# Kernel tuning notes

Hardware: AMD Instinct MI355X
Metric: run time of the kernel (lower is better)

The kernel has to match this reference:

```python
import jax, jax.numpy as jnp
import numpy as np

B, T, C = 8, 4096, 1024
NH = 64          # module sets self.n_head = dim_head = 64
HD = C // NH     # 16


def setup_inputs() -> dict:
    key = jax.random.key(0)
    ks = jax.random.split(key, 9)
    s = 1.0 / np.sqrt(C).astype(np.float32)
    x = jax.random.normal(ks[0], (B, T, C), jnp.float32)
    Wq = jax.random.normal(ks[1], (C, C), jnp.float32) * s
    bq = jax.random.normal(ks[2], (C,), jnp.float32) * 0.01
    Wk = jax.random.normal(ks[3], (C, C), jnp.float32) * s
    bk = jax.random.normal(ks[4], (C,), jnp.float32) * 0.01
    Wv = jax.random.normal(ks[5], (C, C), jnp.float32) * s
    bv = jax.random.normal(ks[6], (C,), jnp.float32) * 0.01
    Wp = jax.random.normal(ks[7], (C, C), jnp.float32) * s
    bp = jax.random.normal(ks[8], (C,), jnp.float32) * 0.01
    return {"x": x, "Wq": Wq, "bq": bq, "Wk": Wk, "bk": bk,
            "Wv": Wv, "bv": bv, "Wp": Wp, "bp": bp}


def _heads(t):
    # [B, T, C] -> [B, NH, T, HD]
    return t.reshape(B, T, NH, HD).transpose(0, 2, 1, 3)


def reference(x, Wq, bq, Wk, bk, Wv, bv, Wp, bp):
    # self-attention path: y = x; kv_mask=None (masked path is unreachable in source)
    q = _heads(x @ Wq.T + bq)
    k = _heads(x @ Wk.T + bk)
    v = _heads(x @ Wv.T + bv)
    q = jax.nn.softmax(q, axis=-1)
    k = jax.nn.softmax(k, axis=-1)
    k_cumsum = k.sum(axis=2, keepdims=True)               # [B, NH, 1, HD]
    D_inv = 1.0 / (q * k_cumsum).sum(axis=-1, keepdims=True)  # [B, NH, T, 1]
    context = jnp.einsum('bhtd,bhte->bhde', k, v)          # [B, NH, HD, HD]
    y = jnp.einsum('bhtd,bhde->bhte', q, context) * D_inv  # [B, NH, T, HD]
    y = y.transpose(0, 2, 1, 3).reshape(B, T, C)           # b h n d -> b n (h d)
    return y @ Wp.T + bp
```

## Files before the change

kernel.cpp:

```cpp
#include <hip/hip_runtime.h>
#include <stdint.h>


typedef __attribute__((ext_vector_type(8))) __bf16 bf16x8;
typedef __attribute__((ext_vector_type(4))) float f32x4;
typedef __attribute__((ext_vector_type(4))) unsigned int u32x4;
typedef __attribute__((ext_vector_type(4))) unsigned short u16x4;

#define AS1 __attribute__((address_space(1)))
#define AS3 __attribute__((address_space(3)))

__device__ __forceinline__ unsigned short f2bf(float f) {
  unsigned int u = __builtin_bit_cast(unsigned int, f);
  u += 0x7FFFu + ((u >> 16) & 1u);
  return (unsigned short)(u >> 16);
}

__device__ __forceinline__ void gl_lds16(const unsigned short* g, unsigned short* l) {
  __builtin_amdgcn_global_load_lds((const AS1 unsigned int*)g, (AS3 unsigned int*)l, 16, 0, 0);
}

__global__ __launch_bounds__(256)
void cvt_all(const float* __restrict__ x,
             const float* __restrict__ w0, const float* __restrict__ w1,
             const float* __restrict__ w2, const float* __restrict__ w3,
             unsigned short* __restrict__ xb, unsigned short* __restrict__ wb) {
  const int blk = blockIdx.x;
  if (blk < 2048) {
    int i = blk * 256 + threadIdx.x;
    #pragma unroll 4
    for (; i < 8388608; i += 524288) {
      f32x4 v = *(const f32x4*)(x + (size_t)i * 4);
      u16x4 o;
      o.x = f2bf(v.x); o.y = f2bf(v.y); o.z = f2bf(v.z); o.w = f2bf(v.w);
      *(u16x4*)(xb + (size_t)i * 4) = o;
    }
  } else {
    const int g = (blk - 2048) * 256 + threadIdx.x;
    const int w = g >> 17;
    const int r = g & 131071;
    const int f = r >> 6;
    const int l = r & 63;
    const int n = (f >> 5) * 16 + (l & 15);
    const int k = (f & 31) * 32 + (l >> 4) * 8;
    const float* ws[4] = {w0, w1, w2, w3};
    const float* src = ws[w] + (size_t)n * 1024 + k;
    f32x4 v0 = *(const f32x4*)src;
    f32x4 v1 = *(const f32x4*)(src + 4);
    u16x4 a, b;
    a.x = f2bf(v0.x); a.y = f2bf(v0.y); a.z = f2bf(v0.z); a.w = f2bf(v0.w);
    b.x = f2bf(v1.x); b.y = f2bf(v1.y); b.z = f2bf(v1.z); b.w = f2bf(v1.w);
    unsigned short* o = wb + (size_t)g * 8;
    *(u16x4*)o = a;
    *(u16x4*)(o + 4) = b;
  }
}

template<int KIND>
__global__ __launch_bounds__(256, 3)
void gemm_pipe(const unsigned short* __restrict__ A,
               const unsigned short* __restrict__ Wf,
               const float* __restrict__ b0, const float* __restrict__ b1,
               const float* __restrict__ b2,
               unsigned short* __restrict__ oq, unsigned short* __restrict__ okT,
               unsigned short* __restrict__ ovT, float* __restrict__ of)
{
  __shared__ __align__(16) unsigned short lds[24576];

  const int tid  = threadIdx.x;
  const int lane = tid & 63;
  const int wid  = tid >> 6;

  const int flat  = blockIdx.x;
  const int xcd   = flat & 7;
  const int i     = flat >> 3;
  const int bcg   = i >> 8;
  const int r     = i & 255;
  const int panel = r >> 3;
  const int c     = r & 7;
  const int brow  = (xcd * 32 + panel) * 128;
  const int bcol  = (bcg * 8 + c) * 128;

  const int srow = wid * 16 + (lane >> 2);
  const int scol = ((lane & 3) ^ ((lane >> 3) & 3)) << 3;
  const unsigned short* a_src = A + (size_t)(brow + srow) * 1024 + scol;
  unsigned short* Ldst = lds + wid * 512;

  const int wm = (wid >> 1) * 64;
  const int wn = (wid & 1) * 64;
  const int fr = lane & 15;
  const int fg = lane >> 4;
  const int aoff = (wm + fr) * 32 + ((fg ^ ((fr >> 1) & 3)) << 3);

  const unsigned short* wfp = Wf + ((size_t)((bcol + wn) >> 4) * 32) * 512 + lane * 8;

  const f32x4 fz = {0.f, 0.f, 0.f, 0.f};
  f32x4 acc[4][4];
  #pragma unroll
  for (int mt = 0; mt < 4; ++mt)
    #pragma unroll
    for (int nt = 0; nt < 4; ++nt) acc[mt][nt] = fz;

  auto stage = [&](int T, int sb) {
    unsigned short* d = Ldst + sb * 8192;
    const unsigned short* g = a_src + T * 64;
    gl_lds16(g,              d);
    gl_lds16(g + 65536,      d + 2048);
    gl_lds16(g + 32,         d + 4096);
    gl_lds16(g + 65536 + 32, d + 6144);
  };
  auto loadB = [&](int k32, bf16x8 (&dst)[4]) {
    #pragma unroll
    for (int nt = 0; nt < 4; ++nt)
      dst[nt] = __builtin_bit_cast(bf16x8,
        *(const u32x4*)(wfp + (size_t)k32 * 512 + (size_t)nt * 16384));
  };

  bf16x8 bEven[4], bOdd[4];

  stage(0, 0); stage(1, 1);
  loadB(0, bEven);
  asm volatile("s_waitcnt vmcnt(8)" ::: "memory");
  __builtin_amdgcn_sched_barrier(0);
  __builtin_amdgcn_s_barrier();

  for (int T = 0; T < 16; ++T) {
    const unsigned short* Lb = lds + (T % 3) * 8192;
    bf16x8 af[8];
    #pragma unroll
    for (int mt = 0; mt < 4; ++mt) {
      af[mt]     = __builtin_bit_cast(bf16x8, *(const u32x4*)&Lb[aoff + mt * 512]);
      af[4 + mt] = __builtin_bit_cast(bf16x8, *(const u32x4*)&Lb[4096 + aoff + mt * 512]);
    }
    asm volatile("s_waitcnt lgkmcnt(0)" ::: "memory");
    __builtin_amdgcn_sched_barrier(0);
    if (T + 2 < 16) stage(T + 2, (T + 2) % 3);
    loadB(2 * T + 1, bOdd);
    if (T <= 13)      asm volatile("s_waitcnt vmcnt(8)" ::: "memory");
    else              asm volatile("s_waitcnt vmcnt(4)" ::: "memory");
    __builtin_amdgcn_sched_barrier(0);
    if (T < 15) __builtin_amdgcn_s_barrier();

    __builtin_amdgcn_s_setprio(1);
    #pragma unroll
    for (int mt = 0; mt < 4; ++mt)
      #pragma unroll
      for (int nt = 0; nt < 4; ++nt)
        acc[mt][nt] = __builtin_amdgcn_mfma_f32_16x16x32_bf16(af[mt], bEven[nt], acc[mt][nt], 0, 0, 0);
    __builtin_amdgcn_s_setprio(0);

    if (T <= 14) loadB(2 * T + 2, bEven);
    if (T <= 13)      asm volatile("s_waitcnt vmcnt(8)" ::: "memory");
    else if (T == 14) asm volatile("s_waitcnt vmcnt(4)" ::: "memory");
    else              asm volatile("s_waitcnt vmcnt(0)" ::: "memory");
    __builtin_amdgcn_sched_barrier(0);

    __builtin_amdgcn_s_setprio(1);
    #pragma unroll
    for (int mt = 0; mt < 4; ++mt)
      #pragma unroll
      for (int nt = 0; nt < 4; ++nt)
        acc[mt][nt] = __builtin_amdgcn_mfma_f32_16x16x32_bf16(af[4 + mt], bOdd[nt], acc[mt][nt], 0, 0, 0);
    __builtin_amdgcn_s_setprio(0);
  }

  const int sec = (KIND == 0) ? (bcol >> 10) : 0;
  const float* bias = (KIND == 1) ? b0 : (sec == 0 ? b0 : (sec == 1 ? b1 : b2));

  #pragma unroll
  for (int nt = 0; nt < 4; ++nt) {
    const int n_glob = bcol + wn + nt * 16 + fr;
    const int nn = (KIND == 0) ? (n_glob & 1023) : n_glob;
    const float bv = bias[nn];
    #pragma unroll
    for (int mt = 0; mt < 4; ++mt) {
      const int m0 = brow + wm + mt * 16 + fg * 4;
      float vals[4];
      #pragma unroll
      for (int r2 = 0; r2 < 4; ++r2) vals[r2] = acc[mt][nt][r2] + bv;

      if (KIND == 0 && sec <= 1) {
        #pragma unroll
        for (int r2 = 0; r2 < 4; ++r2) {
          float e = __expf(vals[r2]);
          float sm = e;
          #pragma unroll
          for (int s = 1; s < 16; s <<= 1) sm += __shfl_xor(sm, s, 64);
          vals[r2] = e * __builtin_amdgcn_rcpf(sm);
        }
      }

      if (KIND == 1) {
        #pragma unroll
        for (int r2 = 0; r2 < 4; ++r2)
          of[(size_t)(m0 + r2) * 1024 + n_glob] = vals[r2];
      } else if (sec == 0) {
        #pragma unroll
        for (int r2 = 0; r2 < 4; ++r2)
          oq[(size_t)(m0 + r2) * 1024 + nn] = f2bf(vals[r2]);
      } else {
        unsigned short* o = (sec == 1) ? okT : ovT;
        const int bb = m0 >> 12;
        const int t0 = m0 & 4095;
        const int hh = nn >> 4;
        const int dd = nn & 15;
        u16x4 pk;
        pk.x = f2bf(vals[0]); pk.y = f2bf(vals[1]);
        pk.z = f2bf(vals[2]); pk.w = f2bf(vals[3]);
        *(u16x4*)&o[(((size_t)bb * 64 + hh) * 16 + dd) * 4096 + t0] = pk;
      }
    }
  }
}

__global__ __launch_bounds__(256)
void attn_kernel(const unsigned short* __restrict__ qb,
                 const unsigned short* __restrict__ kT,
                 const unsigned short* __restrict__ vT,
                 unsigned short* __restrict__ yb)
{
  const int pair = blockIdx.x;
  const int b    = pair >> 5;
  const int hp   = pair & 31;
  const int tid  = threadIdx.x;
  const int lane = tid & 63;
  const int wid  = tid >> 6;
  const int fr   = lane & 15;
  const int fg   = lane >> 4;

  const unsigned short* kT0 = kT + ((size_t)(b * 64 + hp * 2) * 16) * 4096;
  const unsigned short* vT0 = vT + ((size_t)(b * 64 + hp * 2) * 16) * 4096;
  const unsigned short* kT1 = kT0 + 16 * 4096;
  const unsigned short* vT1 = vT0 + 16 * 4096;

  const u32x4 uz = {0u, 0u, 0u, 0u};
  const f32x4 fz = {0.f, 0.f, 0.f, 0.f};
  const u32x4 uo = {0x3F803F80u, 0x3F803F80u, 0x3F803F80u, 0x3F803F80u};
  const bf16x8 ones = __builtin_bit_cast(bf16x8, uo);

  f32x4 cctx0 = fz, ckc0 = fz, cctx1 = fz, ckc1 = fz;
  #pragma unroll 2
  for (int t0 = wid * 1024; t0 < (wid + 1) * 1024; t0 += 32) {
    const size_t off = (size_t)fr * 4096 + t0 + fg * 8;
    bf16x8 ak0 = __builtin_bit_cast(bf16x8, *(const u32x4*)&kT0[off]);
    bf16x8 bv0 = __builtin_bit_cast(bf16x8, *(const u32x4*)&vT0[off]);
    bf16x8 ak1 = __builtin_bit_cast(bf16x8, *(const u32x4*)&kT1[off]);
    bf16x8 bv1 = __builtin_bit_cast(bf16x8, *(const u32x4*)&vT1[off]);
    cctx0 = __builtin_amdgcn_mfma_f32_16x16x32_bf16(ak0, bv0, cctx0, 0, 0, 0);
    ckc0  = __builtin_amdgcn_mfma_f32_16x16x32_bf16(ak0, ones, ckc0, 0, 0, 0);
    cctx1 = __builtin_amdgcn_mfma_f32_16x16x32_bf16(ak1, bv1, cctx1, 0, 0, 0);
    ckc1  = __builtin_amdgcn_mfma_f32_16x16x32_bf16(ak1, ones, ckc1, 0, 0, 0);
  }

  __shared__ float red[4][2][16][16];
  __shared__ float kcr[4][2][16];
  __shared__ float ctxf[2][16][16];
  __shared__ float kcf[2][16];

  #pragma unroll
  for (int r = 0; r < 4; ++r) {
    red[wid][0][fg * 4 + r][fr] = cctx0[r];
    red[wid][1][fg * 4 + r][fr] = cctx1[r];
  }
  if (fr == 0) {
    #pragma unroll
    for (int r = 0; r < 4; ++r) {
      kcr[wid][0][fg * 4 + r] = ckc0[r];
      kcr[wid][1][fg * 4 + r] = ckc1[r];
    }
  }
  __syncthreads();
  {
    const int d = (tid >> 4) & 15, e = tid & 15;
    #pragma unroll
    for (int hh = 0; hh < 2; ++hh)
      ctxf[hh][d][e] = red[0][hh][d][e] + red[1][hh][d][e] + red[2][hh][d][e] + red[3][hh][d][e];
    if (tid < 32) {
      const int hh = tid >> 4, dd = tid & 15;
      kcf[hh][dd] = kcr[0][hh][dd] + kcr[1][hh][dd] + kcr[2][hh][dd] + kcr[3][hh][dd];
    }
  }
  __syncthreads();

  bf16x8 bctx0 = __builtin_bit_cast(bf16x8, uz);
  bf16x8 bctx1 = __builtin_bit_cast(bf16x8, uz);
  bf16x8 bkc0  = __builtin_bit_cast(bf16x8, uz);
  bf16x8 bkc1  = __builtin_bit_cast(bf16x8, uz);
  if (fg < 2) {
    #pragma unroll
    for (int j = 0; j < 8; ++j) {
      const int d = fg * 8 + j;
      bctx0[j] = (__bf16)ctxf[0][d][fr];
      bkc0[j]  = (__bf16)kcf[0][d];
    }
  } else {
    #pragma unroll
    for (int j = 0; j < 8; ++j) {
      const int d = (fg - 2) * 8 + j;
      bctx1[j] = (__bf16)ctxf[1][d][fr];
      bkc1[j]  = (__bf16)kcf[1][d];
    }
  }

  const size_t cbase = (size_t)b * 4096 * 1024 + (size_t)hp * 32;

  for (int step = 0; step < 64; ++step) {
    const int t0 = step * 64 + wid * 16;
    bf16x8 af = __builtin_bit_cast(bf16x8,
        *(const u32x4*)&qb[cbase + (size_t)(t0 + fr) * 1024 + fg * 8]);
    f32x4 cy0 = __builtin_amdgcn_mfma_f32_16x16x32_bf16(af, bctx0, fz, 0, 0, 0);
    f32x4 cy1 = __builtin_amdgcn_mfma_f32_16x16x32_bf16(af, bctx1, fz, 0, 0, 0);
    f32x4 cd0 = __builtin_amdgcn_mfma_f32_16x16x32_bf16(af, bkc0,  fz, 0, 0, 0);
    f32x4 cd1 = __builtin_amdgcn_mfma_f32_16x16x32_bf16(af, bkc1,  fz, 0, 0, 0);
    #pragma unroll
    for (int r = 0; r < 4; ++r) {
      const int t = t0 + fg * 4 + r;
      const size_t o = cbase + (size_t)t * 1024;
      yb[o + fr]      = f2bf(cy0[r] * __builtin_amdgcn_rcpf(cd0[r]));
      yb[o + 16 + fr] = f2bf(cy1[r] * __builtin_amdgcn_rcpf(cd1[r]));
    }
  }
}

extern "C" void kernel_launch(void* const* d_in, const int* in_sizes, int n_in,
                              void* d_out, int out_size, void* d_ws, size_t ws_size,
                              hipStream_t stream)
{
  (void)in_sizes; (void)n_in; (void)out_size; (void)ws_size;
  const float* x  = (const float*)d_in[0];
  const float* Wq = (const float*)d_in[1];
  const float* bq = (const float*)d_in[2];
  const float* Wk = (const float*)d_in[3];
  const float* bk = (const float*)d_in[4];
  const float* Wv = (const float*)d_in[5];
  const float* bv = (const float*)d_in[6];
  const float* Wp = (const float*)d_in[7];
  const float* bp = (const float*)d_in[8];

  char* ws = (char*)d_ws;
  unsigned short* xb  = (unsigned short*)(ws);
  unsigned short* wb  = (unsigned short*)(ws + 67108864);
  unsigned short* qb  = (unsigned short*)(ws + 75497472);
  unsigned short* kTb = (unsigned short*)(ws + 142606336);
  unsigned short* vTb = (unsigned short*)(ws + 209715200);

  cvt_all<<<4096, 256, 0, stream>>>(x, Wq, Wk, Wv, Wp, xb, wb);

  gemm_pipe<0><<<6144, 256, 0, stream>>>(xb, wb, bq, bk, bv, qb, kTb, vTb, nullptr);

  attn_kernel<<<256, 256, 0, stream>>>(qb, kTb, vTb, xb );

  gemm_pipe<1><<<2048, 256, 0, stream>>>(xb , wb + 3145728, bp, bp, bp,
                                         nullptr, nullptr, nullptr, (float*)d_out);
}
```

Measured before the change: 453.2 us.

## Switch projection GEMMs from 16x16x32 to 32x32x16 bf16 MFMA tiles

The GEMM inner loop now issues 32x32x16 bf16 MFMAs on 2x2 tiles of 16-float accumulators per wave, replacing 4x4 tiles of 16x16x32 MFMAs. The weight pre-conversion kernel writes a new 32-row-by-16-k fragment layout to match, and the LDS A-fragment offsets and swizzle are rewritten for 32-lane row groups. The epilogue is reworked for the 32x32 accumulator row mapping, including the per-head softmax shuffle and the transposed K/V stores. The goal is fewer MFMA issues and better operand reuse per instruction. The cost is a more scattered epilogue store pattern and new LDS access offsets that may cause bank conflicts.

```diff
diff --git a/kernel.cpp b/kernel.cpp
--- a/kernel.cpp
+++ b/kernel.cpp
@@ -4,6 +4,7 @@
 
 typedef __attribute__((ext_vector_type(8))) __bf16 bf16x8;
 typedef __attribute__((ext_vector_type(4))) float f32x4;
+typedef __attribute__((ext_vector_type(16))) float f32x16;
 typedef __attribute__((ext_vector_type(4))) unsigned int u32x4;
 typedef __attribute__((ext_vector_type(4))) unsigned short u16x4;
 
@@ -41,8 +42,8 @@
     const int r = g & 131071;
     const int f = r >> 6;
     const int l = r & 63;
-    const int n = (f >> 5) * 16 + (l & 15);
-    const int k = (f & 31) * 32 + (l >> 4) * 8;
+    const int n = (f >> 6) * 32 + (l & 31);
+    const int k = (f & 63) * 16 + (l >> 5) * 8;
     const float* ws[4] = {w0, w1, w2, w3};
     const float* src = ws[w] + (size_t)n * 1024 + k;
     f32x4 v0 = *(const f32x4*)src;
@@ -86,20 +87,24 @@
   const unsigned short* a_src = A + (size_t)(brow + srow) * 1024 + scol;
   unsigned short* Ldst = lds + wid * 512;
 
-  const int wm = (wid >> 1) * 64;
-  const int wn = (wid & 1) * 64;
-  const int fr = lane & 15;
-  const int fg = lane >> 4;
-  const int aoff = (wm + fr) * 32 + ((fg ^ ((fr >> 1) & 3)) << 3);
-
-  const unsigned short* wfp = Wf + ((size_t)((bcol + wn) >> 4) * 32) * 512 + lane * 8;
-
-  const f32x4 fz = {0.f, 0.f, 0.f, 0.f};
-  f32x4 acc[4][4];
+  const int wm  = (wid >> 1) * 64;
+  const int wn  = (wid & 1) * 64;
+  const int l31 = lane & 31;
+  const int ln5 = lane >> 5;
+
+  const char* aBase = (const char*)lds + (size_t)(wm + l31) * 64;
+  const int s00 = ((ln5 ^ ((lane >> 1) & 3)) << 4);
+  const int s01 = s00 ^ 32;
+
+  const unsigned short* wfp = Wf + ((size_t)((bcol + wn) >> 5) * 64) * 512 + lane * 8;
+
+  f32x16 acc[2][2];
   #pragma unroll
-  for (int mt = 0; mt < 4; ++mt)
-    #pragma unroll
-    for (int nt = 0; nt < 4; ++nt) acc[mt][nt] = fz;
+  for (int mf = 0; mf < 2; ++mf)
+    #pragma unroll
+    for (int nf = 0; nf < 2; ++nf)
+      #pragma unroll
+      for (int e = 0; e < 16; ++e) acc[mf][nf][e] = 0.f;
 
   auto stage = [&](int T, int sb) {
     unsigned short* d = Ldst + sb * 8192;
@@ -109,11 +114,13 @@
     gl_lds16(g + 32,         d + 4096);
     gl_lds16(g + 65536 + 32, d + 6144);
   };
-  auto loadB = [&](int k32, bf16x8 (&dst)[4]) {
-    #pragma unroll
-    for (int nt = 0; nt < 4; ++nt)
-      dst[nt] = __builtin_bit_cast(bf16x8,
-        *(const u32x4*)(wfp + (size_t)k32 * 512 + (size_t)nt * 16384));
+  auto loadB = [&](int kstep, bf16x8 (&dst)[4]) {
+    #pragma unroll
+    for (int nf = 0; nf < 2; ++nf)
+      #pragma unroll
+      for (int j = 0; j < 2; ++j)
+        dst[nf * 2 + j] = __builtin_bit_cast(bf16x8,
+          *(const u32x4*)(wfp + (size_t)(nf * 64 + kstep + j) * 512));
   };
 
   bf16x8 bEven[4], bOdd[4];
@@ -125,17 +132,20 @@
   __builtin_amdgcn_s_barrier();
 
   for (int T = 0; T < 16; ++T) {
-    const unsigned short* Lb = lds + (T % 3) * 8192;
+    const char* Lb = aBase + (T % 3) * 16384;
     bf16x8 af[8];
     #pragma unroll
-    for (int mt = 0; mt < 4; ++mt) {
-      af[mt]     = __builtin_bit_cast(bf16x8, *(const u32x4*)&Lb[aoff + mt * 512]);
-      af[4 + mt] = __builtin_bit_cast(bf16x8, *(const u32x4*)&Lb[4096 + aoff + mt * 512]);
+    for (int mf = 0; mf < 2; ++mf) {
+      const char* base = Lb + mf * 2048;
+      af[mf * 4 + 0] = __builtin_bit_cast(bf16x8, *(const u32x4*)(base + s00));
+      af[mf * 4 + 1] = __builtin_bit_cast(bf16x8, *(const u32x4*)(base + s01));
+      af[mf * 4 + 2] = __builtin_bit_cast(bf16x8, *(const u32x4*)(base + 8192 + s00));
+      af[mf * 4 + 3] = __builtin_bit_cast(bf16x8, *(const u32x4*)(base + 8192 + s01));
     }
     asm volatile("s_waitcnt lgkmcnt(0)" ::: "memory");
     __builtin_amdgcn_sched_barrier(0);
     if (T + 2 < 16) stage(T + 2, (T + 2) % 3);
-    loadB(2 * T + 1, bOdd);
+    loadB(4 * T + 2, bOdd);
     if (T <= 13)      asm volatile("s_waitcnt vmcnt(8)" ::: "memory");
     else              asm volatile("s_waitcnt vmcnt(4)" ::: "memory");
     __builtin_amdgcn_sched_barrier(0);
@@ -143,13 +153,15 @@
 
     __builtin_amdgcn_s_setprio(1);
     #pragma unroll
-    for (int mt = 0; mt < 4; ++mt)
-      #pragma unroll
-      for (int nt = 0; nt < 4; ++nt)
-        acc[mt][nt] = __builtin_amdgcn_mfma_f32_16x16x32_bf16(af[mt], bEven[nt], acc[mt][nt], 0, 0, 0);
+    for (int mf = 0; mf < 2; ++mf)
+      #pragma unroll
+      for (int nf = 0; nf < 2; ++nf) {
+        acc[mf][nf] = __builtin_amdgcn_mfma_f32_32x32x16_bf16(af[mf * 4 + 0], bEven[nf * 2 + 0], acc[mf][nf], 0, 0, 0);
+        acc[mf][nf] = __builtin_amdgcn_mfma_f32_32x32x16_bf16(af[mf * 4 + 1], bEven[nf * 2 + 1], acc[mf][nf], 0, 0, 0);
+      }
     __builtin_amdgcn_s_setprio(0);
 
-    if (T <= 14) loadB(2 * T + 2, bEven);
+    if (T <= 14) loadB(4 * (T + 1), bEven);
     if (T <= 13)      asm volatile("s_waitcnt vmcnt(8)" ::: "memory");
     else if (T == 14) asm volatile("s_waitcnt vmcnt(4)" ::: "memory");
     else              asm volatile("s_waitcnt vmcnt(0)" ::: "memory");
@@ -157,10 +169,12 @@
 
     __builtin_amdgcn_s_setprio(1);
     #pragma unroll
-    for (int mt = 0; mt < 4; ++mt)
-      #pragma unroll
-      for (int nt = 0; nt < 4; ++nt)
-        acc[mt][nt] = __builtin_amdgcn_mfma_f32_16x16x32_bf16(af[4 + mt], bOdd[nt], acc[mt][nt], 0, 0, 0);
+    for (int mf = 0; mf < 2; ++mf)
+      #pragma unroll
+      for (int nf = 0; nf < 2; ++nf) {
+        acc[mf][nf] = __builtin_amdgcn_mfma_f32_32x32x16_bf16(af[mf * 4 + 2], bOdd[nf * 2 + 0], acc[mf][nf], 0, 0, 0);
+        acc[mf][nf] = __builtin_amdgcn_mfma_f32_32x32x16_bf16(af[mf * 4 + 3], bOdd[nf * 2 + 1], acc[mf][nf], 0, 0, 0);
+      }
     __builtin_amdgcn_s_setprio(0);
   }
 
@@ -168,20 +182,19 @@
   const float* bias = (KIND == 1) ? b0 : (sec == 0 ? b0 : (sec == 1 ? b1 : b2));
 
   #pragma unroll
-  for (int nt = 0; nt < 4; ++nt) {
-    const int n_glob = bcol + wn + nt * 16 + fr;
+  for (int nf = 0; nf < 2; ++nf) {
+    const int n_glob = bcol + wn + nf * 32 + l31;
     const int nn = (KIND == 0) ? (n_glob & 1023) : n_glob;
     const float bv = bias[nn];
     #pragma unroll
-    for (int mt = 0; mt < 4; ++mt) {
-      const int m0 = brow + wm + mt * 16 + fg * 4;
-      float vals[4];
-      #pragma unroll
-      for (int r2 = 0; r2 < 4; ++r2) vals[r2] = acc[mt][nt][r2] + bv;
+    for (int mf = 0; mf < 2; ++mf) {
+      float vals[16];
+      #pragma unroll
+      for (int r2 = 0; r2 < 16; ++r2) vals[r2] = acc[mf][nf][r2] + bv;
 
       if (KIND == 0 && sec <= 1) {
         #pragma unroll
-        for (int r2 = 0; r2 < 4; ++r2) {
+        for (int r2 = 0; r2 < 16; ++r2) {
           float e = __expf(vals[r2]);
           float sm = e;
           #pragma unroll
@@ -192,22 +205,30 @@
 
       if (KIND == 1) {
         #pragma unroll
-        for (int r2 = 0; r2 < 4; ++r2)
-          of[(size_t)(m0 + r2) * 1024 + n_glob] = vals[r2];
+        for (int r2 = 0; r2 < 16; ++r2) {
+          const int m = brow + wm + mf * 32 + (r2 & 3) + 8 * (r2 >> 2) + 4 * ln5;
+          of[(size_t)m * 1024 + n_glob] = vals[r2];
+        }
       } else if (sec == 0) {
         #pragma unroll
-        for (int r2 = 0; r2 < 4; ++r2)
-          oq[(size_t)(m0 + r2) * 1024 + nn] = f2bf(vals[r2]);
+        for (int r2 = 0; r2 < 16; ++r2) {
+          const int m = brow + wm + mf * 32 + (r2 & 3) + 8 * (r2 >> 2) + 4 * ln5;
+          oq[(size_t)m * 1024 + nn] = f2bf(vals[r2]);
+        }
       } else {
         unsigned short* o = (sec == 1) ? okT : ovT;
-        const int bb = m0 >> 12;
-        const int t0 = m0 & 4095;
         const int hh = nn >> 4;
         const int dd = nn & 15;
-        u16x4 pk;
-        pk.x = f2bf(vals[0]); pk.y = f2bf(vals[1]);
-        pk.z = f2bf(vals[2]); pk.w = f2bf(vals[3]);
-        *(u16x4*)&o[(((size_t)bb * 64 + hh) * 16 + dd) * 4096 + t0] = pk;
+        #pragma unroll
+        for (int rc = 0; rc < 4; ++rc) {
+          const int m0 = brow + wm + mf * 32 + rc * 8 + 4 * ln5;
+          const int bb = m0 >> 12;
+          const int t0 = m0 & 4095;
+          u16x4 pk;
+          pk.x = f2bf(vals[rc * 4 + 0]); pk.y = f2bf(vals[rc * 4 + 1]);
+          pk.z = f2bf(vals[rc * 4 + 2]); pk.w = f2bf(vals[rc * 4 + 3]);
+          *(u16x4*)&o[(((size_t)bb * 64 + hh) * 16 + dd) * 4096 + t0] = pk;
+        }
       }
     }
   }
```

New measurement: 480.9 us. 1.06x slower.
